# Kernel optimization log

Hardware: AMD Instinct MI355X
Metric: run time of the kernel (lower is better)

The kernel has to match this reference:

```python
import jax, jax.numpy as jnp
import numpy as np
import math

B, S, D_EMB = 1, 4096, 768
N_HEADS, D_QKV = 12, 64
INV_TEMP = 1.0


def setup_inputs() -> dict:
    key = jax.random.key(0)
    ks = jax.random.split(key, 11)
    s = 0.02
    return {
        "q_in": jax.random.normal(ks[0], (B, S, D_EMB), jnp.float32),
        "k_in": jax.random.normal(ks[1], (B, S, D_EMB), jnp.float32),
        "v_in": jax.random.normal(ks[2], (B, S, D_EMB), jnp.float32),
        "W_q": jax.random.normal(ks[3], (D_EMB, N_HEADS * D_QKV), jnp.float32) * s,
        "b_q": jnp.zeros((N_HEADS * D_QKV,), jnp.float32),
        "W_k": jax.random.normal(ks[4], (D_EMB, N_HEADS * D_QKV), jnp.float32) * s,
        "b_k": jnp.zeros((N_HEADS * D_QKV,), jnp.float32),
        "W_v": jax.random.normal(ks[5], (D_EMB, N_HEADS * D_QKV), jnp.float32) * s,
        "b_v": jnp.zeros((N_HEADS * D_QKV,), jnp.float32),
        "W_o": jax.random.normal(ks[6], (N_HEADS * D_QKV, D_EMB), jnp.float32) * s,
        "b_o": jnp.zeros((D_EMB,), jnp.float32),
    }


def _split_heads(x):  # [B,S,H*D] -> [B,H,S,D]
    b, s, _ = x.shape
    return x.reshape(b, s, N_HEADS, D_QKV).transpose(0, 2, 1, 3)


def reference(q_in, k_in, v_in, W_q, b_q, W_k, b_k, W_v, b_v, W_o, b_o):
    q = _split_heads(q_in @ W_q + b_q)
    k = _split_heads(k_in @ W_k + b_k)
    v = _split_heads(v_in @ W_v + b_v)
    # full [B,H,S,S] score matrix (module materializes it for custom masking)
    scores = INV_TEMP * jnp.einsum('bhqd,bhkd->bhqk', q, k) / math.sqrt(D_QKV)
    attn = jax.nn.softmax(scores, axis=-1)
    out = jnp.einsum('bhqk,bhkd->bhqd', attn, v)  # [B,H,S,D]
    out = out.transpose(0, 2, 1, 3).reshape(q_in.shape[0], q_in.shape[1], N_HEADS * D_QKV)
    return out @ W_o + b_o
```

## Files before the change

### kernel.cpp

```cpp
#include <hip/hip_runtime.h>

#define S 4096
#define E 768
#define NH 12
#define DH 64
#define QSCALE (0.125f * 1.44269504f)
#define KSPLIT 4

typedef __bf16 bf16;
typedef __bf16 bf16x4 __attribute__((ext_vector_type(4)));
typedef __bf16 bf16x8 __attribute__((ext_vector_type(8)));
typedef float  f32x4  __attribute__((ext_vector_type(4)));

__device__ __forceinline__ void async16(const bf16* g, bf16* l) {
  __builtin_amdgcn_global_load_lds(
      (const __attribute__((address_space(1))) void*)g,
      (__attribute__((address_space(3))) void*)l, 16, 0, 0);
}

__global__ __launch_bounds__(256) void cast3(const float* __restrict__ i0,
                                             const float* __restrict__ i1,
                                             const float* __restrict__ i2,
                                             bf16* __restrict__ o0,
                                             bf16* __restrict__ o1,
                                             bf16* __restrict__ o2) {
  const float* in = blockIdx.z == 0 ? i0 : (blockIdx.z == 1 ? i1 : i2);
  bf16* out = blockIdx.z == 0 ? o0 : (blockIdx.z == 1 ? o1 : o2);
  int i = (blockIdx.x * blockDim.x + threadIdx.x) * 4;
  float4 v = *(const float4*)(in + i);
  bf16x4 o = { (bf16)v.x, (bf16)v.y, (bf16)v.z, (bf16)v.w };
  *(bf16x4*)(out + i) = o;
}

__global__ __launch_bounds__(256) void transpose4(const float* __restrict__ w0,
                                                  const float* __restrict__ w1,
                                                  const float* __restrict__ w2,
                                                  const float* __restrict__ w3,
                                                  bf16* __restrict__ t0,
                                                  bf16* __restrict__ t1,
                                                  bf16* __restrict__ t2,
                                                  bf16* __restrict__ t3) {
  const float* W = blockIdx.z == 0 ? w0 : (blockIdx.z == 1 ? w1 : (blockIdx.z == 2 ? w2 : w3));
  bf16* Wt = blockIdx.z == 0 ? t0 : (blockIdx.z == 1 ? t1 : (blockIdx.z == 2 ? t2 : t3));
  __shared__ float t[32][33];
  const int tx = threadIdx.x, ty = threadIdx.y;
  const int x = blockIdx.x * 32 + tx;
  const int y0 = blockIdx.y * 32;
  for (int j = ty; j < 32; j += 8)
    t[j][tx] = W[(y0 + j) * E + x];
  __syncthreads();
  for (int j = ty; j < 32; j += 8)
    Wt[(blockIdx.x * 32 + j) * E + y0 + tx] = (bf16)t[tx][j];
}

__global__ __launch_bounds__(256) void gemm128(const bf16* __restrict__ A0,
                                               const bf16* __restrict__ A1,
                                               const bf16* __restrict__ A2,
                                               const bf16* __restrict__ B0,
                                               const bf16* __restrict__ B1,
                                               const bf16* __restrict__ B2,
                                               const float* __restrict__ bias0,
                                               const float* __restrict__ bias1,
                                               const float* __restrict__ bias2,
                                               bf16* __restrict__ C0,
                                               bf16* __restrict__ C1,
                                               bf16* __restrict__ C2) {
  __shared__ __align__(16) bf16 smem[128 * 136];
  bf16* Asm = smem;
  bf16* Bsm = smem + 4096;
  bf16* Cs  = smem;

  const int z = blockIdx.z;
  const bf16* A  = z == 0 ? A0 : (z == 1 ? A1 : A2);
  const bf16* Bt = z == 0 ? B0 : (z == 1 ? B1 : B2);
  const float* bias = z == 0 ? bias0 : (z == 1 ? bias1 : bias2);

  const int tid = threadIdx.x;
  const int wv = tid >> 6, lane = tid & 63;
  const int quad = lane >> 4, l16 = lane & 15;
  const int m0 = blockIdx.x * 128, n0 = blockIdx.y * 128;
  const int wm = (wv >> 1) * 64, wn = (wv & 1) * 64;
  const int srow = lane >> 2, scol = (lane & 3) * 8;

  f32x4 acc[4][4] = {};

  for (int k0 = 0; k0 < E; k0 += 32) {
#pragma unroll
    for (int j = 0; j < 2; j++) {
      const int ch = wv * 2 + j;
      async16(&A[(size_t)(m0 + ch * 16 + srow) * E + k0 + scol], &Asm[ch * 512]);
      async16(&Bt[(size_t)(n0 + ch * 16 + srow) * E + k0 + scol], &Bsm[ch * 512]);
    }
    __syncthreads();
    bf16x8 af[4], bfv[4];
#pragma unroll
    for (int mi = 0; mi < 4; mi++)
      af[mi] = *(const bf16x8*)&Asm[(wm + mi * 16 + l16) * 32 + quad * 8];
#pragma unroll
    for (int ni = 0; ni < 4; ni++)
      bfv[ni] = *(const bf16x8*)&Bsm[(wn + ni * 16 + l16) * 32 + quad * 8];
#pragma unroll
    for (int mi = 0; mi < 4; mi++)
#pragma unroll
      for (int ni = 0; ni < 4; ni++)
        acc[mi][ni] = __builtin_amdgcn_mfma_f32_16x16x32_bf16(af[mi], bfv[ni], acc[mi][ni], 0, 0, 0);
    __syncthreads();
  }

  const float scale = (z == 0) ? QSCALE : 1.0f;
#pragma unroll
  for (int mi = 0; mi < 4; mi++) {
#pragma unroll
    for (int ni = 0; ni < 4; ni++) {
      const int nl = wn + ni * 16 + l16;
      const float bv = bias[n0 + nl];
#pragma unroll
      for (int r = 0; r < 4; r++) {
        const int ml = wm + mi * 16 + quad * 4 + r;
        const float v = (acc[mi][ni][r] + bv) * scale;
        if (z == 2) Cs[nl * 136 + ml] = (bf16)v;
        else        Cs[ml * 136 + nl] = (bf16)v;
      }
    }
  }
  __syncthreads();

  if (z == 0) {
    const int e = lane & 7;
#pragma unroll
    for (int p = 0; p < 8; p++) {
      const int hr = p * 32 + wv * 8 + (lane >> 3);
      const int r = hr >> 1, hf = hr & 1;
      bf16x8 c = *(const bf16x8*)&Cs[r * 136 + hf * 64 + e * 8];
      *(bf16x8*)(C0 + (size_t)((n0 >> 6) + hf) * S * DH + (size_t)(m0 + r) * DH + e * 8) = c;
    }
  } else {
    bf16* dst = (z == 1) ? C1 : C2;
    const int quadc = lane >> 4, l16c = lane & 15;
#pragma unroll
    for (int p = 0; p < 8; p++) {
      const int cid = p * 4 + wv;
      const int reg = cid >> 3;
      const int i = cid & 7;
      const int h_l = reg >> 1, tile = reg & 1;
      bf16x8 c;
      if (z == 1) {
        const int row = tile * 64 + (i >> 1) * 16 + l16c;
        const int col = h_l * 64 + (i & 1) * 32 + quadc * 8;
        c = *(const bf16x8*)&Cs[row * 136 + col];
      } else {
        const int nl = h_l * 64 + (i >> 1) * 16 + l16c;
        const int ml = tile * 64 + (i & 1) * 32 + quadc * 8;
        c = *(const bf16x8*)&Cs[nl * 136 + ml];
      }
      *(bf16x8*)(dst + (size_t)((n0 >> 6) + h_l) * S * DH +
                 (size_t)((m0 >> 6) + tile) * 4096 + i * 512 + lane * 8) = c;
    }
  }
}

__global__ __launch_bounds__(256, 4) void attn(const bf16* __restrict__ Q,
                                               const bf16* __restrict__ Kf,
                                               const bf16* __restrict__ Vf,
                                               bf16* __restrict__ Op0,
                                               bf16* __restrict__ Op1,
                                               bf16* __restrict__ Op2,
                                               bf16* __restrict__ Op3,
                                               float* __restrict__ Lp) {
  __shared__ bf16 P[4][32][76];
  const int h = blockIdx.y, ks = blockIdx.z;
  const int tid = threadIdx.x;
  const int wave = tid >> 6, lane = tid & 63;
  const int quad = lane >> 4, l16 = lane & 15;
  const int q0 = blockIdx.x * 128 + wave * 32;

  const bf16* Qh  = Q  + (size_t)h * S * DH;
  const bf16* Kfh = Kf + (size_t)h * S * DH;
  const bf16* Vfh = Vf + (size_t)h * S * DH;
  bf16* Op = ks == 0 ? Op0 : (ks == 1 ? Op1 : (ks == 2 ? Op2 : Op3));

  bf16x8 aq[2][2];
#pragma unroll
  for (int mi = 0; mi < 2; mi++)
#pragma unroll
    for (int j = 0; j < 2; j++)
      aq[mi][j] = *(const bf16x8*)&Qh[(size_t)(q0 + mi * 16 + l16) * DH + j * 32 + quad * 8];

  bf16x8 ones;
#pragma unroll
  for (int e = 0; e < 8; e++) ones[e] = (bf16)1.0f;

  f32x4 o[4][2] = {};
  f32x4 ol[2] = {};

  const bf16* kptr = Kfh + (size_t)ks * (S / KSPLIT) * DH + lane * 8;
  const bf16* vptr = Vfh + (size_t)ks * (S / KSPLIT) * DH + lane * 8;

  for (int it = 0; it < S / KSPLIT / 64; ++it, kptr += 4096, vptr += 4096) {
    bf16x8 kr[8];
#pragma unroll
    for (int i = 0; i < 8; i++) kr[i] = *(const bf16x8*)(kptr + i * 512);

#pragma unroll
    for (int mi = 0; mi < 2; mi++) {
      f32x4 sfr[4] = {};
#pragma unroll
      for (int nb = 0; nb < 4; nb++) {
        sfr[nb] = __builtin_amdgcn_mfma_f32_16x16x32_bf16(aq[mi][0], kr[nb * 2], sfr[nb], 0, 0, 0);
        sfr[nb] = __builtin_amdgcn_mfma_f32_16x16x32_bf16(aq[mi][1], kr[nb * 2 + 1], sfr[nb], 0, 0, 0);
      }
#pragma unroll
      for (int nb = 0; nb < 4; nb++)
#pragma unroll
        for (int r = 0; r < 4; r++)
          P[wave][mi * 16 + quad * 4 + r][nb * 16 + l16] = (bf16)__builtin_exp2f(sfr[nb][r]);
    }

    bf16x8 vr[8];
#pragma unroll
    for (int i = 0; i < 8; i++) vr[i] = *(const bf16x8*)(vptr + i * 512);

    bf16x8 ap[2][2];
#pragma unroll
    for (int mi = 0; mi < 2; mi++)
#pragma unroll
      for (int j = 0; j < 2; j++)
        ap[mi][j] = *(const bf16x8*)&P[wave][mi * 16 + l16][j * 32 + quad * 8];

#pragma unroll
    for (int mi = 0; mi < 2; mi++) {
      ol[mi] = __builtin_amdgcn_mfma_f32_16x16x32_bf16(ap[mi][0], ones, ol[mi], 0, 0, 0);
      ol[mi] = __builtin_amdgcn_mfma_f32_16x16x32_bf16(ap[mi][1], ones, ol[mi], 0, 0, 0);
    }
#pragma unroll
    for (int db = 0; db < 4; db++)
#pragma unroll
      for (int mi = 0; mi < 2; mi++) {
        o[db][mi] = __builtin_amdgcn_mfma_f32_16x16x32_bf16(ap[mi][0], vr[db * 2], o[db][mi], 0, 0, 0);
        o[db][mi] = __builtin_amdgcn_mfma_f32_16x16x32_bf16(ap[mi][1], vr[db * 2 + 1], o[db][mi], 0, 0, 0);
      }
  }

  float* Lph = Lp + (size_t)(ks * NH + h) * S;
  if (l16 == 0) {
#pragma unroll
    for (int mi = 0; mi < 2; mi++)
#pragma unroll
      for (int r = 0; r < 4; r++)
        Lph[q0 + mi * 16 + quad * 4 + r] = ol[mi][r];
  }
#pragma unroll
  for (int db = 0; db < 4; db++) {
    const int d = db * 16 + l16;
#pragma unroll
    for (int mi = 0; mi < 2; mi++)
#pragma unroll
      for (int r = 0; r < 4; r++) {
        const int row = q0 + mi * 16 + quad * 4 + r;
        Op[(size_t)row * E + h * DH + d] = (bf16)o[db][mi][r];
      }
  }
}

__global__ __launch_bounds__(256) void combine(const bf16* __restrict__ Op0,
                                               const bf16* __restrict__ Op1,
                                               const bf16* __restrict__ Op2,
                                               const bf16* __restrict__ Op3,
                                               const float* __restrict__ Lp,
                                               bf16* __restrict__ Obf) {
  const int i8 = blockIdx.x * 256 + threadIdx.x;
  const size_t base = (size_t)i8 * 8;
  const int row = (int)(base / E), c = (int)(base % E);
  const int h = c >> 6;
  const float l = Lp[(size_t)h * S + row] + Lp[(size_t)(NH + h) * S + row] +
                  Lp[(size_t)(2 * NH + h) * S + row] + Lp[(size_t)(3 * NH + h) * S + row];
  const float rl = 1.0f / l;
  bf16x8 a = *(const bf16x8*)(Op0 + base);
  bf16x8 b = *(const bf16x8*)(Op1 + base);
  bf16x8 cc = *(const bf16x8*)(Op2 + base);
  bf16x8 d = *(const bf16x8*)(Op3 + base);
  bf16x8 o;
#pragma unroll
  for (int e = 0; e < 8; e++)
    o[e] = (bf16)((((float)a[e] + (float)b[e]) + ((float)cc[e] + (float)d[e])) * rl);
  *(bf16x8*)(Obf + base) = o;
}

__global__ __launch_bounds__(256) void gemm64(const bf16* __restrict__ A,
                                              const bf16* __restrict__ Bt,
                                              const float* __restrict__ bias,
                                              float* __restrict__ C) {
  __shared__ __align__(16) bf16 Asm[64 * 32];
  __shared__ __align__(16) bf16 Bsm[64 * 32];
  const int tid = threadIdx.x;
  const int wv = tid >> 6, lane = tid & 63;
  const int quad = lane >> 4, l16 = lane & 15;
  const int m0 = blockIdx.x * 64, n0 = blockIdx.y * 64;
  const int srow = lane >> 2, scol = (lane & 3) * 8;

  f32x4 acc[4] = {};

  for (int k0 = 0; k0 < E; k0 += 32) {
    async16(&A[(size_t)(m0 + wv * 16 + srow) * E + k0 + scol], &Asm[wv * 512]);
    async16(&Bt[(size_t)(n0 + wv * 16 + srow) * E + k0 + scol], &Bsm[wv * 512]);
    __syncthreads();
    bf16x8 af = *(const bf16x8*)&Asm[(wv * 16 + l16) * 32 + quad * 8];
#pragma unroll
    for (int ni = 0; ni < 4; ni++) {
      bf16x8 bfr = *(const bf16x8*)&Bsm[(ni * 16 + l16) * 32 + quad * 8];
      acc[ni] = __builtin_amdgcn_mfma_f32_16x16x32_bf16(af, bfr, acc[ni], 0, 0, 0);
    }
    __syncthreads();
  }

  const int row0 = m0 + wv * 16 + quad * 4;
#pragma unroll
  for (int ni = 0; ni < 4; ni++) {
    const int col = n0 + ni * 16 + l16;
    const float bv = bias[col];
#pragma unroll
    for (int r = 0; r < 4; r++)
      C[(size_t)(row0 + r) * E + col] = acc[ni][r] + bv;
  }
}

extern "C" void kernel_launch(void* const* d_in, const int* in_sizes, int n_in,
                              void* d_out, int out_size, void* d_ws, size_t ws_size,
                              hipStream_t stream) {
  (void)in_sizes; (void)n_in; (void)out_size; (void)ws_size;
  const float* q_in = (const float*)d_in[0];
  const float* k_in = (const float*)d_in[1];
  const float* v_in = (const float*)d_in[2];
  const float* W_q  = (const float*)d_in[3];
  const float* b_q  = (const float*)d_in[4];
  const float* W_k  = (const float*)d_in[5];
  const float* b_k  = (const float*)d_in[6];
  const float* W_v  = (const float*)d_in[7];
  const float* b_v  = (const float*)d_in[8];
  const float* W_o  = (const float*)d_in[9];
  const float* b_o  = (const float*)d_in[10];

  const size_t SE2 = (size_t)S * E * 2;
  const size_t EE2 = (size_t)E * E * 2;
  char* ws = (char*)d_ws;
  bf16* qb  = (bf16*)(ws);
  bf16* kb  = (bf16*)(ws + SE2);
  bf16* vb  = (bf16*)(ws + 2 * SE2);
  bf16* WqT = (bf16*)(ws + 3 * SE2);
  bf16* WkT = (bf16*)(ws + 3 * SE2 + EE2);
  bf16* WvT = (bf16*)(ws + 3 * SE2 + 2 * EE2);
  bf16* WoT = (bf16*)(ws + 3 * SE2 + 3 * EE2);
  bf16* Qh  = (bf16*)(ws + 3 * SE2 + 4 * EE2);
  bf16* Kf  = (bf16*)(ws + 4 * SE2 + 4 * EE2);
  bf16* Vf  = (bf16*)(ws + 5 * SE2 + 4 * EE2);
  bf16* Obf = (bf16*)(ws + 6 * SE2 + 4 * EE2);
  bf16* Op1 = qb;
  bf16* Op2 = kb;
  bf16* Op3 = vb;
  float* Lp = (float*)WqT;

  cast3<<<dim3(S * E / 1024, 1, 3), 256, 0, stream>>>(q_in, k_in, v_in, qb, kb, vb);
  transpose4<<<dim3(24, 24, 4), dim3(32, 8), 0, stream>>>(W_q, W_k, W_v, W_o,
                                                          WqT, WkT, WvT, WoT);

  gemm128<<<dim3(S / 128, E / 128, 3), 256, 0, stream>>>(
      qb, kb, vb, WqT, WkT, WvT, b_q, b_k, b_v, Qh, Kf, Vf);

  attn<<<dim3(S / 128, NH, KSPLIT), 256, 0, stream>>>(Qh, Kf, Vf, Obf, Op1, Op2, Op3, Lp);

  combine<<<dim3(S * E / 2048), 256, 0, stream>>>(Obf, Op1, Op2, Op3, Lp, Obf);

  gemm64<<<dim3(S / 64, E / 64), 256, 0, stream>>>(Obf, WoT, b_o, (float*)d_out);
}
```

Measured before the change: 239.4 us.

## Fuse prologue kernels, retile QKV GEMM, halve attention split, split-K output GEMM

Merges the cast and weight-transpose kernels into one launch. Retiles the QKV GEMM to 128x64 tiles, one head per block, for more blocks. Reduces the attention key split from 4 to 2, double-buffers K fragments in registers, streams V per block and lowers launch bounds to 3 blocks per SM. The output GEMM is split along K into two halves accumulated with atomics into an output that the combine kernel zeroes first. The aim is fewer launches, less partial-sum traffic and better occupancy. The cost is nondeterministic float atomics and longer per-block attention loops.

```diff
diff --git a/kernel.cpp b/kernel.cpp
--- a/kernel.cpp
+++ b/kernel.cpp
@@ -5,67 +5,73 @@
 #define NH 12
 #define DH 64
 #define QSCALE (0.125f * 1.44269504f)
-#define KSPLIT 4
+#define KSPLIT 2
 
 typedef __bf16 bf16;
 typedef __bf16 bf16x4 __attribute__((ext_vector_type(4)));
 typedef __bf16 bf16x8 __attribute__((ext_vector_type(8)));
 typedef float  f32x4  __attribute__((ext_vector_type(4)));
 
+#define MFMA(a, b, c) __builtin_amdgcn_mfma_f32_16x16x32_bf16(a, b, c, 0, 0, 0)
+
 __device__ __forceinline__ void async16(const bf16* g, bf16* l) {
   __builtin_amdgcn_global_load_lds(
       (const __attribute__((address_space(1))) void*)g,
       (__attribute__((address_space(3))) void*)l, 16, 0, 0);
 }
 
-__global__ __launch_bounds__(256) void cast3(const float* __restrict__ i0,
-                                             const float* __restrict__ i1,
-                                             const float* __restrict__ i2,
-                                             bf16* __restrict__ o0,
-                                             bf16* __restrict__ o1,
-                                             bf16* __restrict__ o2) {
-  const float* in = blockIdx.z == 0 ? i0 : (blockIdx.z == 1 ? i1 : i2);
-  bf16* out = blockIdx.z == 0 ? o0 : (blockIdx.z == 1 ? o1 : o2);
-  int i = (blockIdx.x * blockDim.x + threadIdx.x) * 4;
-  float4 v = *(const float4*)(in + i);
-  bf16x4 o = { (bf16)v.x, (bf16)v.y, (bf16)v.z, (bf16)v.w };
-  *(bf16x4*)(out + i) = o;
-}
-
-__global__ __launch_bounds__(256) void transpose4(const float* __restrict__ w0,
-                                                  const float* __restrict__ w1,
-                                                  const float* __restrict__ w2,
-                                                  const float* __restrict__ w3,
-                                                  bf16* __restrict__ t0,
-                                                  bf16* __restrict__ t1,
-                                                  bf16* __restrict__ t2,
-                                                  bf16* __restrict__ t3) {
-  const float* W = blockIdx.z == 0 ? w0 : (blockIdx.z == 1 ? w1 : (blockIdx.z == 2 ? w2 : w3));
-  bf16* Wt = blockIdx.z == 0 ? t0 : (blockIdx.z == 1 ? t1 : (blockIdx.z == 2 ? t2 : t3));
-  __shared__ float t[32][33];
-  const int tx = threadIdx.x, ty = threadIdx.y;
-  const int x = blockIdx.x * 32 + tx;
-  const int y0 = blockIdx.y * 32;
-  for (int j = ty; j < 32; j += 8)
-    t[j][tx] = W[(y0 + j) * E + x];
-  __syncthreads();
-  for (int j = ty; j < 32; j += 8)
-    Wt[(blockIdx.x * 32 + j) * E + y0 + tx] = (bf16)t[tx][j];
-}
-
-__global__ __launch_bounds__(256) void gemm128(const bf16* __restrict__ A0,
-                                               const bf16* __restrict__ A1,
-                                               const bf16* __restrict__ A2,
-                                               const bf16* __restrict__ B0,
-                                               const bf16* __restrict__ B1,
-                                               const bf16* __restrict__ B2,
-                                               const float* __restrict__ bias0,
-                                               const float* __restrict__ bias1,
-                                               const float* __restrict__ bias2,
-                                               bf16* __restrict__ C0,
-                                               bf16* __restrict__ C1,
-                                               bf16* __restrict__ C2) {
-  __shared__ __align__(16) bf16 smem[128 * 136];
+__global__ __launch_bounds__(256) void prologue(const float* __restrict__ q_in,
+                                                const float* __restrict__ k_in,
+                                                const float* __restrict__ v_in,
+                                                const float* __restrict__ w0,
+                                                const float* __restrict__ w1,
+                                                const float* __restrict__ w2,
+                                                const float* __restrict__ w3,
+                                                bf16* __restrict__ qb,
+                                                bf16* __restrict__ kb,
+                                                bf16* __restrict__ vb,
+                                                bf16* __restrict__ t0,
+                                                bf16* __restrict__ t1,
+                                                bf16* __restrict__ t2,
+                                                bf16* __restrict__ t3) {
+  const int bid = blockIdx.x, tid = threadIdx.x;
+  if (bid < 2304) {
+    const int z = bid / 576, rem = bid % 576;
+    const int bx = rem % 24, by = rem / 24;
+    const float* W = z == 0 ? w0 : (z == 1 ? w1 : (z == 2 ? w2 : w3));
+    bf16* Wt = z == 0 ? t0 : (z == 1 ? t1 : (z == 2 ? t2 : t3));
+    __shared__ float t[32][33];
+    const int tx = tid & 31, ty = tid >> 5;
+    for (int j = ty; j < 32; j += 8)
+      t[j][tx] = W[(by * 32 + j) * E + bx * 32 + tx];
+    __syncthreads();
+    for (int j = ty; j < 32; j += 8)
+      Wt[(bx * 32 + j) * E + by * 32 + tx] = (bf16)t[tx][j];
+  } else {
+    const int b2 = bid - 2304;
+    const int z = b2 / 3072, r2 = b2 % 3072;
+    const float* in = z == 0 ? q_in : (z == 1 ? k_in : v_in);
+    bf16* out = z == 0 ? qb : (z == 1 ? kb : vb);
+    const int i = r2 * 1024 + tid * 4;
+    float4 v = *(const float4*)(in + i);
+    bf16x4 o = { (bf16)v.x, (bf16)v.y, (bf16)v.z, (bf16)v.w };
+    *(bf16x4*)(out + i) = o;
+  }
+}
+
+__global__ __launch_bounds__(256) void gemm_qkv(const bf16* __restrict__ A0,
+                                                const bf16* __restrict__ A1,
+                                                const bf16* __restrict__ A2,
+                                                const bf16* __restrict__ B0,
+                                                const bf16* __restrict__ B1,
+                                                const bf16* __restrict__ B2,
+                                                const float* __restrict__ bias0,
+                                                const float* __restrict__ bias1,
+                                                const float* __restrict__ bias2,
+                                                bf16* __restrict__ C0,
+                                                bf16* __restrict__ C1,
+                                                bf16* __restrict__ C2) {
+  __shared__ __align__(16) bf16 smem[9216];
   bf16* Asm = smem;
   bf16* Bsm = smem + 4096;
   bf16* Cs  = smem;
@@ -76,96 +82,85 @@
   const float* bias = z == 0 ? bias0 : (z == 1 ? bias1 : bias2);
 
   const int tid = threadIdx.x;
-  const int wv = tid >> 6, lane = tid & 63;
+  const int w = tid >> 6, lane = tid & 63;
   const int quad = lane >> 4, l16 = lane & 15;
-  const int m0 = blockIdx.x * 128, n0 = blockIdx.y * 128;
-  const int wm = (wv >> 1) * 64, wn = (wv & 1) * 64;
+  const int m0 = blockIdx.x * 128;
+  const int h = blockIdx.y;
+  const int n0 = h * 64;
   const int srow = lane >> 2, scol = (lane & 3) * 8;
 
-  f32x4 acc[4][4] = {};
+  f32x4 acc[2][4] = {};
 
   for (int k0 = 0; k0 < E; k0 += 32) {
 #pragma unroll
     for (int j = 0; j < 2; j++) {
-      const int ch = wv * 2 + j;
+      const int ch = w * 2 + j;
       async16(&A[(size_t)(m0 + ch * 16 + srow) * E + k0 + scol], &Asm[ch * 512]);
-      async16(&Bt[(size_t)(n0 + ch * 16 + srow) * E + k0 + scol], &Bsm[ch * 512]);
-    }
-    __syncthreads();
-    bf16x8 af[4], bfv[4];
-#pragma unroll
-    for (int mi = 0; mi < 4; mi++)
-      af[mi] = *(const bf16x8*)&Asm[(wm + mi * 16 + l16) * 32 + quad * 8];
+    }
+    async16(&Bt[(size_t)(n0 + w * 16 + srow) * E + k0 + scol], &Bsm[w * 512]);
+    __syncthreads();
+    bf16x8 af[2], bfv[4];
+#pragma unroll
+    for (int mi = 0; mi < 2; mi++)
+      af[mi] = *(const bf16x8*)&Asm[(w * 32 + mi * 16 + l16) * 32 + quad * 8];
 #pragma unroll
     for (int ni = 0; ni < 4; ni++)
-      bfv[ni] = *(const bf16x8*)&Bsm[(wn + ni * 16 + l16) * 32 + quad * 8];
-#pragma unroll
-    for (int mi = 0; mi < 4; mi++)
+      bfv[ni] = *(const bf16x8*)&Bsm[(ni * 16 + l16) * 32 + quad * 8];
+#pragma unroll
+    for (int mi = 0; mi < 2; mi++)
 #pragma unroll
       for (int ni = 0; ni < 4; ni++)
-        acc[mi][ni] = __builtin_amdgcn_mfma_f32_16x16x32_bf16(af[mi], bfv[ni], acc[mi][ni], 0, 0, 0);
+        acc[mi][ni] = MFMA(af[mi], bfv[ni], acc[mi][ni]);
     __syncthreads();
   }
 
   const float scale = (z == 0) ? QSCALE : 1.0f;
 #pragma unroll
-  for (int mi = 0; mi < 4; mi++) {
+  for (int mi = 0; mi < 2; mi++) {
 #pragma unroll
     for (int ni = 0; ni < 4; ni++) {
-      const int nl = wn + ni * 16 + l16;
+      const int nl = ni * 16 + l16;
       const float bv = bias[n0 + nl];
 #pragma unroll
       for (int r = 0; r < 4; r++) {
-        const int ml = wm + mi * 16 + quad * 4 + r;
+        const int ml = w * 32 + mi * 16 + quad * 4 + r;
         const float v = (acc[mi][ni][r] + bv) * scale;
         if (z == 2) Cs[nl * 136 + ml] = (bf16)v;
-        else        Cs[ml * 136 + nl] = (bf16)v;
+        else        Cs[ml * 72 + nl] = (bf16)v;
       }
     }
   }
   __syncthreads();
 
   if (z == 0) {
-    const int e = lane & 7;
-#pragma unroll
-    for (int p = 0; p < 8; p++) {
-      const int hr = p * 32 + wv * 8 + (lane >> 3);
-      const int r = hr >> 1, hf = hr & 1;
-      bf16x8 c = *(const bf16x8*)&Cs[r * 136 + hf * 64 + e * 8];
-      *(bf16x8*)(C0 + (size_t)((n0 >> 6) + hf) * S * DH + (size_t)(m0 + r) * DH + e * 8) = c;
+    const int e = (lane & 7) * 8;
+#pragma unroll
+    for (int p = 0; p < 4; p++) {
+      const int row = p * 32 + w * 8 + (lane >> 3);
+      bf16x8 c = *(const bf16x8*)&Cs[row * 72 + e];
+      *(bf16x8*)(C0 + (size_t)h * S * DH + (size_t)(m0 + row) * DH + e) = c;
     }
   } else {
     bf16* dst = (z == 1) ? C1 : C2;
-    const int quadc = lane >> 4, l16c = lane & 15;
-#pragma unroll
-    for (int p = 0; p < 8; p++) {
-      const int cid = p * 4 + wv;
-      const int reg = cid >> 3;
-      const int i = cid & 7;
-      const int h_l = reg >> 1, tile = reg & 1;
+#pragma unroll
+    for (int p = 0; p < 4; p++) {
+      const int fid = p * 4 + w;
+      const int t = fid >> 3, i = fid & 7;
       bf16x8 c;
-      if (z == 1) {
-        const int row = tile * 64 + (i >> 1) * 16 + l16c;
-        const int col = h_l * 64 + (i & 1) * 32 + quadc * 8;
-        c = *(const bf16x8*)&Cs[row * 136 + col];
-      } else {
-        const int nl = h_l * 64 + (i >> 1) * 16 + l16c;
-        const int ml = tile * 64 + (i & 1) * 32 + quadc * 8;
-        c = *(const bf16x8*)&Cs[nl * 136 + ml];
-      }
-      *(bf16x8*)(dst + (size_t)((n0 >> 6) + h_l) * S * DH +
-                 (size_t)((m0 >> 6) + tile) * 4096 + i * 512 + lane * 8) = c;
-    }
-  }
-}
-
-__global__ __launch_bounds__(256, 4) void attn(const bf16* __restrict__ Q,
+      if (z == 1)
+        c = *(const bf16x8*)&Cs[(t * 64 + (i >> 1) * 16 + l16) * 72 + (i & 1) * 32 + quad * 8];
+      else
+        c = *(const bf16x8*)&Cs[((i >> 1) * 16 + l16) * 136 + t * 64 + (i & 1) * 32 + quad * 8];
+      *(bf16x8*)(dst + (size_t)h * S * DH + (size_t)((m0 >> 6) + t) * 4096 + i * 512 + lane * 8) = c;
+    }
+  }
+}
+
+__global__ __launch_bounds__(256, 3) void attn(const bf16* __restrict__ Q,
                                                const bf16* __restrict__ Kf,
                                                const bf16* __restrict__ Vf,
                                                bf16* __restrict__ Op0,
                                                bf16* __restrict__ Op1,
-                                               bf16* __restrict__ Op2,
-                                               bf16* __restrict__ Op3,
                                                float* __restrict__ Lp) {
   __shared__ bf16 P[4][32][76];
   const int h = blockIdx.y, ks = blockIdx.z;
@@ -175,9 +170,9 @@
   const int q0 = blockIdx.x * 128 + wave * 32;
 
   const bf16* Qh  = Q  + (size_t)h * S * DH;
-  const bf16* Kfh = Kf + (size_t)h * S * DH;
-  const bf16* Vfh = Vf + (size_t)h * S * DH;
-  bf16* Op = ks == 0 ? Op0 : (ks == 1 ? Op1 : (ks == 2 ? Op2 : Op3));
+  const bf16* kbase = Kf + (size_t)h * S * DH + (size_t)ks * (S / KSPLIT) * DH + lane * 8;
+  const bf16* vbase = Vf + (size_t)h * S * DH + (size_t)ks * (S / KSPLIT) * DH + lane * 8;
+  bf16* Op = ks ? Op1 : Op0;
 
   bf16x8 aq[2][2];
 #pragma unroll
@@ -193,52 +188,66 @@
   f32x4 o[4][2] = {};
   f32x4 ol[2] = {};
 
-  const bf16* kptr = Kfh + (size_t)ks * (S / KSPLIT) * DH + lane * 8;
-  const bf16* vptr = Vfh + (size_t)ks * (S / KSPLIT) * DH + lane * 8;
-
-  for (int it = 0; it < S / KSPLIT / 64; ++it, kptr += 4096, vptr += 4096) {
-    bf16x8 kr[8];
-#pragma unroll
-    for (int i = 0; i < 8; i++) kr[i] = *(const bf16x8*)(kptr + i * 512);
-
-#pragma unroll
-    for (int mi = 0; mi < 2; mi++) {
-      f32x4 sfr[4] = {};
-#pragma unroll
-      for (int nb = 0; nb < 4; nb++) {
-        sfr[nb] = __builtin_amdgcn_mfma_f32_16x16x32_bf16(aq[mi][0], kr[nb * 2], sfr[nb], 0, 0, 0);
-        sfr[nb] = __builtin_amdgcn_mfma_f32_16x16x32_bf16(aq[mi][1], kr[nb * 2 + 1], sfr[nb], 0, 0, 0);
-      }
-#pragma unroll
-      for (int nb = 0; nb < 4; nb++)
-#pragma unroll
-        for (int r = 0; r < 4; r++)
-          P[wave][mi * 16 + quad * 4 + r][nb * 16 + l16] = (bf16)__builtin_exp2f(sfr[nb][r]);
-    }
-
-    bf16x8 vr[8];
-#pragma unroll
-    for (int i = 0; i < 8; i++) vr[i] = *(const bf16x8*)(vptr + i * 512);
-
-    bf16x8 ap[2][2];
-#pragma unroll
-    for (int mi = 0; mi < 2; mi++)
-#pragma unroll
-      for (int j = 0; j < 2; j++)
-        ap[mi][j] = *(const bf16x8*)&P[wave][mi * 16 + l16][j * 32 + quad * 8];
-
-#pragma unroll
-    for (int mi = 0; mi < 2; mi++) {
-      ol[mi] = __builtin_amdgcn_mfma_f32_16x16x32_bf16(ap[mi][0], ones, ol[mi], 0, 0, 0);
-      ol[mi] = __builtin_amdgcn_mfma_f32_16x16x32_bf16(ap[mi][1], ones, ol[mi], 0, 0, 0);
-    }
-#pragma unroll
-    for (int db = 0; db < 4; db++)
-#pragma unroll
-      for (int mi = 0; mi < 2; mi++) {
-        o[db][mi] = __builtin_amdgcn_mfma_f32_16x16x32_bf16(ap[mi][0], vr[db * 2], o[db][mi], 0, 0, 0);
-        o[db][mi] = __builtin_amdgcn_mfma_f32_16x16x32_bf16(ap[mi][1], vr[db * 2 + 1], o[db][mi], 0, 0, 0);
-      }
+  bf16x8 kr0[8], kr1[8];
+#pragma unroll
+  for (int i = 0; i < 8; i++) kr0[i] = *(const bf16x8*)(kbase + i * 512);
+
+#define ATTN_BODY(T, KR)                                                        \
+  {                                                                             \
+    const bf16* vp = vbase + (T) * 4096;                                        \
+    bf16x8 vr[2];                                                               \
+    f32x4 sfr[4] = {};                                                          \
+    _Pragma("unroll")                                                           \
+    for (int nb = 0; nb < 4; nb++) {                                            \
+      sfr[nb] = MFMA(aq[0][0], KR[nb * 2], sfr[nb]);                            \
+      sfr[nb] = MFMA(aq[0][1], KR[nb * 2 + 1], sfr[nb]);                        \
+    }                                                                           \
+    _Pragma("unroll")                                                           \
+    for (int nb = 0; nb < 4; nb++)                                              \
+      _Pragma("unroll")                                                         \
+      for (int r = 0; r < 4; r++)                                               \
+        P[wave][quad * 4 + r][nb * 16 + l16] = (bf16)__builtin_exp2f(sfr[nb][r]);\
+    _Pragma("unroll")                                                           \
+    for (int nb = 0; nb < 4; nb++) {                                            \
+      f32x4 s2 = {};                                                            \
+      s2 = MFMA(aq[1][0], KR[nb * 2], s2);                                      \
+      s2 = MFMA(aq[1][1], KR[nb * 2 + 1], s2);                                  \
+      _Pragma("unroll")                                                         \
+      for (int r = 0; r < 4; r++)                                               \
+        P[wave][16 + quad * 4 + r][nb * 16 + l16] = (bf16)__builtin_exp2f(s2[r]);\
+    }                                                                           \
+    bf16x8 ap[2][2];                                                            \
+    _Pragma("unroll")                                                           \
+    for (int mi = 0; mi < 2; mi++)                                              \
+      _Pragma("unroll")                                                         \
+      for (int j = 0; j < 2; j++)                                               \
+        ap[mi][j] = *(const bf16x8*)&P[wave][mi * 16 + l16][j * 32 + quad * 8]; \
+    _Pragma("unroll")                                                           \
+    for (int mi = 0; mi < 2; mi++) {                                            \
+      ol[mi] = MFMA(ap[mi][0], ones, ol[mi]);                                   \
+      ol[mi] = MFMA(ap[mi][1], ones, ol[mi]);                                   \
+    }                                                                           \
+    _Pragma("unroll")                                                           \
+    for (int db = 0; db < 4; db++) {                                            \
+      vr[0] = *(const bf16x8*)(vp + (db * 2) * 512);                            \
+      vr[1] = *(const bf16x8*)(vp + (db * 2 + 1) * 512);                        \
+      _Pragma("unroll")                                                         \
+      for (int mi = 0; mi < 2; mi++) {                                          \
+        o[db][mi] = MFMA(ap[mi][0], vr[0], o[db][mi]);                          \
+        o[db][mi] = MFMA(ap[mi][1], vr[1], o[db][mi]);                          \
+      }                                                                         \
+    }                                                                           \
+  }
+
+  for (int it2 = 0; it2 < (S / KSPLIT / 128); ++it2) {
+    const int t0 = it2 * 2, t1 = t0 + 1;
+    const int t2n = (t1 + 1 < S / KSPLIT / 64) ? t1 + 1 : 0;
+#pragma unroll
+    for (int i = 0; i < 8; i++) kr1[i] = *(const bf16x8*)(kbase + t1 * 4096 + i * 512);
+    ATTN_BODY(t0, kr0)
+#pragma unroll
+    for (int i = 0; i < 8; i++) kr0[i] = *(const bf16x8*)(kbase + t2n * 4096 + i * 512);
+    ATTN_BODY(t1, kr1)
   }
 
   float* Lph = Lp + (size_t)(ks * NH + h) * S;
@@ -264,63 +273,62 @@
 
 __global__ __launch_bounds__(256) void combine(const bf16* __restrict__ Op0,
                                                const bf16* __restrict__ Op1,
-                                               const bf16* __restrict__ Op2,
-                                               const bf16* __restrict__ Op3,
                                                const float* __restrict__ Lp,
-                                               bf16* __restrict__ Obf) {
+                                               bf16* __restrict__ Obf,
+                                               float* __restrict__ dout) {
   const int i8 = blockIdx.x * 256 + threadIdx.x;
   const size_t base = (size_t)i8 * 8;
   const int row = (int)(base / E), c = (int)(base % E);
   const int h = c >> 6;
-  const float l = Lp[(size_t)h * S + row] + Lp[(size_t)(NH + h) * S + row] +
-                  Lp[(size_t)(2 * NH + h) * S + row] + Lp[(size_t)(3 * NH + h) * S + row];
+  const float l = Lp[(size_t)h * S + row] + Lp[(size_t)(NH + h) * S + row];
   const float rl = 1.0f / l;
   bf16x8 a = *(const bf16x8*)(Op0 + base);
   bf16x8 b = *(const bf16x8*)(Op1 + base);
-  bf16x8 cc = *(const bf16x8*)(Op2 + base);
-  bf16x8 d = *(const bf16x8*)(Op3 + base);
   bf16x8 o;
 #pragma unroll
-  for (int e = 0; e < 8; e++)
-    o[e] = (bf16)((((float)a[e] + (float)b[e]) + ((float)cc[e] + (float)d[e])) * rl);
+  for (int e = 0; e < 8; e++) o[e] = (bf16)(((float)a[e] + (float)b[e]) * rl);
   *(bf16x8*)(Obf + base) = o;
-}
-
-__global__ __launch_bounds__(256) void gemm64(const bf16* __restrict__ A,
-                                              const bf16* __restrict__ Bt,
-                                              const float* __restrict__ bias,
-                                              float* __restrict__ C) {
+  float4 z = {0.f, 0.f, 0.f, 0.f};
+  *(float4*)(dout + base) = z;
+  *(float4*)(dout + base + 4) = z;
+}
+
+__global__ __launch_bounds__(256) void gemm_final(const bf16* __restrict__ A,
+                                                  const bf16* __restrict__ Bt,
+                                                  const float* __restrict__ bias,
+                                                  float* __restrict__ C) {
   __shared__ __align__(16) bf16 Asm[64 * 32];
   __shared__ __align__(16) bf16 Bsm[64 * 32];
   const int tid = threadIdx.x;
-  const int wv = tid >> 6, lane = tid & 63;
+  const int w = tid >> 6, lane = tid & 63;
   const int quad = lane >> 4, l16 = lane & 15;
   const int m0 = blockIdx.x * 64, n0 = blockIdx.y * 64;
+  const int kbase = blockIdx.z * (E / 2);
   const int srow = lane >> 2, scol = (lane & 3) * 8;
 
   f32x4 acc[4] = {};
 
-  for (int k0 = 0; k0 < E; k0 += 32) {
-    async16(&A[(size_t)(m0 + wv * 16 + srow) * E + k0 + scol], &Asm[wv * 512]);
-    async16(&Bt[(size_t)(n0 + wv * 16 + srow) * E + k0 + scol], &Bsm[wv * 512]);
-    __syncthreads();
-    bf16x8 af = *(const bf16x8*)&Asm[(wv * 16 + l16) * 32 + quad * 8];
+  for (int k0 = kbase; k0 < kbase + E / 2; k0 += 32) {
+    async16(&A[(size_t)(m0 + w * 16 + srow) * E + k0 + scol], &Asm[w * 512]);
+    async16(&Bt[(size_t)(n0 + w * 16 + srow) * E + k0 + scol], &Bsm[w * 512]);
+    __syncthreads();
+    bf16x8 af = *(const bf16x8*)&Asm[(w * 16 + l16) * 32 + quad * 8];
 #pragma unroll
     for (int ni = 0; ni < 4; ni++) {
       bf16x8 bfr = *(const bf16x8*)&Bsm[(ni * 16 + l16) * 32 + quad * 8];
-      acc[ni] = __builtin_amdgcn_mfma_f32_16x16x32_bf16(af, bfr, acc[ni], 0, 0, 0);
-    }
-    __syncthreads();
-  }
-
-  const int row0 = m0 + wv * 16 + quad * 4;
+      acc[ni] = MFMA(af, bfr, acc[ni]);
+    }
+    __syncthreads();
+  }
+
+  const int row0 = m0 + w * 16 + quad * 4;
 #pragma unroll
   for (int ni = 0; ni < 4; ni++) {
     const int col = n0 + ni * 16 + l16;
-    const float bv = bias[col];
+    const float bv = blockIdx.z == 0 ? bias[col] : 0.0f;
 #pragma unroll
     for (int r = 0; r < 4; r++)
-      C[(size_t)(row0 + r) * E + col] = acc[ni][r] + bv;
+      unsafeAtomicAdd(&C[(size_t)(row0 + r) * E + col], acc[ni][r] + bv);
   }
 }
 
@@ -355,20 +363,17 @@
   bf16* Vf  = (bf16*)(ws + 5 * SE2 + 4 * EE2);
   bf16* Obf = (bf16*)(ws + 6 * SE2 + 4 * EE2);
   bf16* Op1 = qb;
-  bf16* Op2 = kb;
-  bf16* Op3 = vb;
   float* Lp = (float*)WqT;
 
-  cast3<<<dim3(S * E / 1024, 1, 3), 256, 0, stream>>>(q_in, k_in, v_in, qb, kb, vb);
-  transpose4<<<dim3(24, 24, 4), dim3(32, 8), 0, stream>>>(W_q, W_k, W_v, W_o,
-                                                          WqT, WkT, WvT, WoT);
-
-  gemm128<<<dim3(S / 128, E / 128, 3), 256, 0, stream>>>(
+  prologue<<<dim3(2304 + 3 * 3072), 256, 0, stream>>>(
+      q_in, k_in, v_in, W_q, W_k, W_v, W_o, qb, kb, vb, WqT, WkT, WvT, WoT);
+
+  gemm_qkv<<<dim3(S / 128, NH, 3), 256, 0, stream>>>(
       qb, kb, vb, WqT, WkT, WvT, b_q, b_k, b_v, Qh, Kf, Vf);
 
-  attn<<<dim3(S / 128, NH, KSPLIT), 256, 0, stream>>>(Qh, Kf, Vf, Obf, Op1, Op2, Op3, Lp);
-
-  combine<<<dim3(S * E / 2048), 256, 0, stream>>>(Obf, Op1, Op2, Op3, Lp, Obf);
-
-  gemm64<<<dim3(S / 64, E / 64), 256, 0, stream>>>(Obf, WoT, b_o, (float*)d_out);
-}
+  attn<<<dim3(S / 128, NH, KSPLIT), 256, 0, stream>>>(Qh, Kf, Vf, Obf, Op1, Lp);
+
+  combine<<<dim3(S * E / 2048), 256, 0, stream>>>(Obf, Op1, Lp, Obf, (float*)d_out);
+
+  gemm_final<<<dim3(S / 64, E / 64, 2), 256, 0, stream>>>(Obf, WoT, b_o, (float*)d_out);
+}
```

Result: slower. 272.7 us (+13.9%).
